# Kernel tuning notes

Hardware: AMD Instinct MI355X
Metric: run time of the kernel (lower is better)

The kernel has to match this reference:

```python
import jax, jax.numpy as jnp
import numpy as np

B, NX, C, KX = 16, 8192, 128, 16  # batch, grid size, channels, retained positive modes


def setup_inputs() -> dict:
    key = jax.random.key(0)
    k1, k2, k3 = jax.random.split(key, 3)
    x = jax.random.normal(k1, (B, NX, C), dtype=jnp.float32)
    scale = 1.0 / (C ** 2)
    w_real = scale * jax.random.uniform(k2, (KX + 1, C, C), dtype=jnp.float32)
    w_imag = scale * jax.random.uniform(k3, (KX + 1, C, C), dtype=jnp.float32)
    return {"x": x, "w_real": w_real, "w_imag": w_imag}


def reference(x, w_real, w_imag):
    # x: (b, nx, c); weights: (kx+1, c, c) complex
    nx = x.shape[1]
    k1 = w_real.shape[0]  # kx + 1 retained frequencies
    w = w_real + 1j * w_imag
    fx = jnp.fft.rfft(x, axis=-2)  # (b, nx//2+1, c) complex
    # torch.matmul(weights, fx[:, :kx+1, :, None])[..., 0]:
    # out[b,k,i] = sum_j w[k,i,j] * fx[b,k,j]
    out_ft = jnp.einsum('kij,bkj->bki', w, fx[:, :k1, :])
    # zero-pad truncated spectrum back to full rfft length, then inverse
    pad = nx // 2 + 1 - k1
    out_full = jnp.pad(out_ft, ((0, 0), (0, pad), (0, 0)))
    return jnp.fft.irfft(out_full, n=nx, axis=-2)
```

## Files before the change

kernel.cpp:

```cpp
#include <hip/hip_runtime.h>
#include <math.h>

#define B_     16
#define NX_    8192
#define C_     128
#define K1_    17
#define KP_    18
#define NC_    64
#define NH_    4096

typedef float v2f __attribute__((ext_vector_type(2)));
typedef float v4f __attribute__((ext_vector_type(4)));

#define GPART_F ((size_t)B_ * K1_ * 2 * NC_ * C_)

__global__ __launch_bounds__(256) void k_fwd(const float* __restrict__ x,
                                             float* __restrict__ ws) {
    __shared__ v4f smem[2 * 64 * 19];

    float* gpart = ws;
    const int b = blockIdx.y;
    const int c = blockIdx.x;
    const int t = threadIdx.x;
    const int jq  = t & 31;
    const int sub = (t >> 5) & 1;
    const int w   = t >> 6;
    const int i0  = c * 64;

    {
        float2* tg = (float2*)smem;
        for (int idx = t; idx < 64 * KP_; idx += 256) {
            int i = idx / KP_;
            int k = idx - i * KP_;
            float2 v = make_float2(0.f, 0.f);
            if (k < K1_) {
                int m = (k * (i0 + i)) & (NX_ - 1);
                float rev = (float)m * (1.0f / (float)NX_);
                v = make_float2(__builtin_amdgcn_cosf(rev),
                                __builtin_amdgcn_sinf(rev));
            }
            tg[idx] = v;
        }
    }
    __syncthreads();

    v4f gr[9], gs[9];
#pragma unroll
    for (int kk = 0; kk < 9; ++kk) { gr[kk] = (v4f)(0.f); gs[kk] = (v4f)(0.f); }

    const size_t xb = (size_t)b * NX_ * C_;
    const int ibase = w * 16;
    const float2* tp = (const float2*)smem + (size_t)ibase * KP_ + sub * 9;
    const float* xlo_p = x + xb + (size_t)(i0 + ibase) * C_ + 4 * jq;
    const float* xhi_p = x + xb + (size_t)(NX_ - (i0 + ibase)) * C_ + 4 * jq;

#pragma unroll 4
    for (int s = 0; s < 16; ++s) {
        const int nlo = i0 + ibase + s;
        v4f xlo = *(const v4f*)(xlo_p + (size_t)s * C_);
        v4f xhi = (v4f)(0.f);
        if (nlo > 0)
            xhi = *(const v4f*)(xhi_p - (size_t)s * C_);
        v4f xp = xlo + xhi;
        v4f xm = xlo - xhi;
        const float2* tr = tp + (size_t)s * KP_;
#pragma unroll
        for (int kk = 0; kk < 9; ++kk) {
            float2 tt = tr[kk];
            gr[kk] = __builtin_elementwise_fma(xp, (v4f)(tt.x), gr[kk]);
            gs[kk] = __builtin_elementwise_fma(xm, (v4f)(tt.y), gs[kk]);
        }
    }

    if (c == 0 && w == 0) {
        v4f x4 = *(const v4f*)(x + xb + (size_t)NH_ * C_ + 4 * jq);
#pragma unroll
        for (int kk = 0; kk < 9; ++kk) {
            int k = sub * 9 + kk;
            gr[kk] += (k & 1) ? -x4 : x4;
        }
    }

    const int lid = t & 63;
    __syncthreads();
    if (w >= 2) {
        v4f* p = smem + ((size_t)(w - 2) * 64 + lid) * 19;
#pragma unroll
        for (int kk = 0; kk < 9; ++kk) { p[2 * kk] = gr[kk]; p[2 * kk + 1] = gs[kk]; }
    }
    __syncthreads();
    if (w < 2) {
        const v4f* p = smem + ((size_t)w * 64 + lid) * 19;
#pragma unroll
        for (int kk = 0; kk < 9; ++kk) { gr[kk] += p[2 * kk]; gs[kk] += p[2 * kk + 1]; }
    }
    __syncthreads();
    if (w == 1) {
        v4f* p = smem + (size_t)lid * 19;
#pragma unroll
        for (int kk = 0; kk < 9; ++kk) { p[2 * kk] = gr[kk]; p[2 * kk + 1] = gs[kk]; }
    }
    __syncthreads();
    if (w == 0) {
        const v4f* p = smem + (size_t)lid * 19;
#pragma unroll
        for (int kk = 0; kk < 9; ++kk) {
            gr[kk] += p[2 * kk];
            gs[kk] += p[2 * kk + 1];
            int k = sub * 9 + kk;
            if (k < K1_) {
                float* gpR = gpart + ((((size_t)b * K1_ + k) * 2 + 0) * NC_ + c) * C_ + 4 * jq;
                float* gpS = gpart + ((((size_t)b * K1_ + k) * 2 + 1) * NC_ + c) * C_ + 4 * jq;
                *(v4f*)gpR = gr[kk];
                *(v4f*)gpS = gs[kk];
            }
        }
    }
}

__global__ __launch_bounds__(1024) void k_mix(const float* __restrict__ wr_g,
                                              const float* __restrict__ wi_g,
                                              float* __restrict__ ws) {
    const int k = blockIdx.x;
    const int b = blockIdx.y;
    const int t = threadIdx.x;

    const float* gpart = ws;
    float2* acoef = (float2*)(ws + GPART_F);

    __shared__ float part[8][C_];
    __shared__ float gsum[2][C_];
    __shared__ float hp[16][C_];

    {
        const int ch = t & 127, ri = (t >> 7) & 1, sh = t >> 8;
        const float* base = gpart
            + (((size_t)b * K1_ + k) * 2 + ri) * ((size_t)NC_ * C_) + ch;
        float g = 0.f;
#pragma unroll
        for (int s = 0; s < 16; ++s) g += base[(size_t)(sh * 16 + s) * C_];
        part[sh * 2 + ri][ch] = g;
    }
    __syncthreads();
    if (t < 256) {
        const int ch = t & 127, ri = t >> 7;
        gsum[ri][ch] = part[ri][ch] + part[2 + ri][ch]
                     + part[4 + ri][ch] + part[6 + ri][ch];
    }
    __syncthreads();

    {
        const int i = t & 127, q = t >> 7;
        float hr = 0.f, hi = 0.f;
        const float* wrp = wr_g + ((size_t)k * C_ + i) * C_;
        const float* wip = wi_g + ((size_t)k * C_ + i) * C_;
#pragma unroll
        for (int jjj = 0; jjj < 16; ++jjj) {
            int jj = q * 16 + jjj;
            float wr = wrp[jj], wi = wip[jj];
            float a = gsum[0][jj], cc = gsum[1][jj];
            hr = fmaf(wr, a, hr); hr = fmaf( wi, cc, hr);
            hi = fmaf(wi, a, hi); hi = fmaf(-wr, cc, hi);
        }
        hp[q * 2 + 0][i] = hr;
        hp[q * 2 + 1][i] = hi;
    }
    __syncthreads();
    if (t < 128) {
        const int i = t;
        float hr = 0.f, hi = 0.f;
#pragma unroll
        for (int q = 0; q < 8; ++q) { hr += hp[q * 2][i]; hi += hp[q * 2 + 1][i]; }
        float cf = (k == 0 ? 1.0f : 2.0f) / (float)NX_;
        acoef[((size_t)b * K1_ + k) * C_ + i] = make_float2(cf * hr, -cf * hi);
    }
}

__global__ __launch_bounds__(256) void k_inv(float* __restrict__ out,
                                             const float* __restrict__ ws) {
    __shared__ float2 smem[64 * K1_];

    const float4* acoef4 = (const float4*)(ws + GPART_F);
    const int b = blockIdx.y;
    const int c = blockIdx.x;
    const int t = threadIdx.x;
    const int jp = t & 63;
    const int h = t >> 6;
    const int i0 = c * 64;

    for (int idx = t; idx < 64 * K1_; idx += 256) {
        int i = idx / K1_;
        int k = idx - i * K1_;
        int m = (k * (i0 + i)) & (NX_ - 1);
        float rev = (float)m * (1.0f / (float)NX_);
        smem[idx] = make_float2(__builtin_amdgcn_cosf(rev),
                                __builtin_amdgcn_sinf(rev));
    }

    v2f arP[K1_], aiP[K1_];
#pragma unroll
    for (int k = 0; k < K1_; ++k) {
        float4 a = acoef4[((size_t)b * K1_ + k) * (C_ / 2) + jp];
        arP[k] = (v2f){a.x, a.z};
        aiP[k] = (v2f){a.y, a.w};
    }
    __syncthreads();

    const size_t ob = (size_t)b * NX_ * C_;
    const float2* tl = smem + (size_t)h * 16 * K1_;
#pragma unroll 4
    for (int s = 0; s < 16; ++s) {
        const int nlo = i0 + h * 16 + s;
        const float2* tr = tl + s * K1_;
        v2f S1 = (v2f)(0.f), S2 = (v2f)(0.f);
#pragma unroll
        for (int k = 0; k < K1_; ++k) {
            float2 tt = tr[k];
            v2f cc = {tt.x, tt.x};
            v2f ss = {tt.y, tt.y};
            S1 = __builtin_elementwise_fma(arP[k], cc, S1);
            S2 = __builtin_elementwise_fma(aiP[k], ss, S2);
        }
        *(v2f*)(out + ob + (size_t)nlo * C_ + 2 * jp) = S1 + S2;
        if (nlo > 0)
            *(v2f*)(out + ob + (size_t)(NX_ - nlo) * C_ + 2 * jp) = S1 - S2;
    }

    if (c == 0 && h == 0) {
        v2f o = (v2f)(0.f);
#pragma unroll
        for (int k = 0; k < K1_; ++k) o += (k & 1) ? -arP[k] : arP[k];
        *(v2f*)(out + ob + (size_t)NH_ * C_ + 2 * jp) = o;
    }
}

extern "C" void kernel_launch(void* const* d_in, const int* in_sizes, int n_in,
                              void* d_out, int out_size, void* d_ws, size_t ws_size,
                              hipStream_t stream) {
    const float* x  = (const float*)d_in[0];
    const float* wr = (const float*)d_in[1];
    const float* wi = (const float*)d_in[2];
    float* out = (float*)d_out;
    float* ws  = (float*)d_ws;

    k_fwd<<<dim3(NC_, B_), 256, 0, stream>>>(x, ws);
    k_mix<<<dim3(K1_, B_), 1024, 0, stream>>>(wr, wi, ws);
    k_inv<<<dim3(NC_, B_), 256, 0, stream>>>(out, ws);
}
```

Measured before the change: 52.90 us.

## Use half-period even/odd mode symmetry instead of mirror symmetry in forward and inverse DFT

The forward and inverse DFT kernels now pair position n with n+NX/2 instead of n with NX-n. Even modes see x[n]+x[n+NX/2] and odd modes see x[n]-x[n+NX/2], so each thread does a single sign-folded combine of two rows and uses the same input for both cos and sin accumulations. The twiddle table is reordered into even/odd mode groups. This removes the nlo>0 branch and the special Nyquist-row fixups, and the stores and loads become contiguous forward strides. The FMA count per element is unchanged, and the mode indexing on write-out is more complex.

```diff
diff --git a/kernel.cpp b/kernel.cpp
--- a/kernel.cpp
+++ b/kernel.cpp
@@ -31,9 +31,10 @@
         float2* tg = (float2*)smem;
         for (int idx = t; idx < 64 * KP_; idx += 256) {
             int i = idx / KP_;
-            int k = idx - i * KP_;
+            int p = idx - i * KP_;
             float2 v = make_float2(0.f, 0.f);
-            if (k < K1_) {
+            if (p < K1_) {
+                int k = (p < 9) ? 2 * p : 2 * (p - 9) + 1;
                 int m = (k * (i0 + i)) & (NX_ - 1);
                 float rev = (float)m * (1.0f / (float)NX_);
                 v = make_float2(__builtin_amdgcn_cosf(rev),
@@ -50,34 +51,22 @@
 
     const size_t xb = (size_t)b * NX_ * C_;
     const int ibase = w * 16;
+    const float sg = sub ? -1.f : 1.f;
     const float2* tp = (const float2*)smem + (size_t)ibase * KP_ + sub * 9;
     const float* xlo_p = x + xb + (size_t)(i0 + ibase) * C_ + 4 * jq;
-    const float* xhi_p = x + xb + (size_t)(NX_ - (i0 + ibase)) * C_ + 4 * jq;
+    const float* xhi_p = xlo_p + (size_t)NH_ * C_;
 
 #pragma unroll 4
     for (int s = 0; s < 16; ++s) {
-        const int nlo = i0 + ibase + s;
         v4f xlo = *(const v4f*)(xlo_p + (size_t)s * C_);
-        v4f xhi = (v4f)(0.f);
-        if (nlo > 0)
-            xhi = *(const v4f*)(xhi_p - (size_t)s * C_);
-        v4f xp = xlo + xhi;
-        v4f xm = xlo - xhi;
+        v4f xhi = *(const v4f*)(xhi_p + (size_t)s * C_);
+        v4f xs = __builtin_elementwise_fma(xhi, (v4f)(sg), xlo);
         const float2* tr = tp + (size_t)s * KP_;
 #pragma unroll
         for (int kk = 0; kk < 9; ++kk) {
             float2 tt = tr[kk];
-            gr[kk] = __builtin_elementwise_fma(xp, (v4f)(tt.x), gr[kk]);
-            gs[kk] = __builtin_elementwise_fma(xm, (v4f)(tt.y), gs[kk]);
-        }
-    }
-
-    if (c == 0 && w == 0) {
-        v4f x4 = *(const v4f*)(x + xb + (size_t)NH_ * C_ + 4 * jq);
-#pragma unroll
-        for (int kk = 0; kk < 9; ++kk) {
-            int k = sub * 9 + kk;
-            gr[kk] += (k & 1) ? -x4 : x4;
+            gr[kk] = __builtin_elementwise_fma(xs, (v4f)(tt.x), gr[kk]);
+            gs[kk] = __builtin_elementwise_fma(xs, (v4f)(tt.y), gs[kk]);
         }
     }
 
@@ -107,8 +96,8 @@
         for (int kk = 0; kk < 9; ++kk) {
             gr[kk] += p[2 * kk];
             gs[kk] += p[2 * kk + 1];
-            int k = sub * 9 + kk;
-            if (k < K1_) {
+            if (sub == 0 || kk < 8) {
+                int k = sub ? 2 * kk + 1 : 2 * kk;
                 float* gpR = gpart + ((((size_t)b * K1_ + k) * 2 + 0) * NC_ + c) * C_ + 4 * jq;
                 float* gpS = gpart + ((((size_t)b * K1_ + k) * 2 + 1) * NC_ + c) * C_ + 4 * jq;
                 *(v4f*)gpR = gr[kk];
@@ -208,29 +197,27 @@
 
     const size_t ob = (size_t)b * NX_ * C_;
     const float2* tl = smem + (size_t)h * 16 * K1_;
+    float* olo = out + ob + (size_t)(i0 + h * 16) * C_ + 2 * jp;
+    float* ohi = olo + (size_t)NH_ * C_;
 #pragma unroll 4
     for (int s = 0; s < 16; ++s) {
-        const int nlo = i0 + h * 16 + s;
         const float2* tr = tl + s * K1_;
-        v2f S1 = (v2f)(0.f), S2 = (v2f)(0.f);
+        v2f Se = (v2f)(0.f), So = (v2f)(0.f);
 #pragma unroll
         for (int k = 0; k < K1_; ++k) {
             float2 tt = tr[k];
             v2f cc = {tt.x, tt.x};
             v2f ss = {tt.y, tt.y};
-            S1 = __builtin_elementwise_fma(arP[k], cc, S1);
-            S2 = __builtin_elementwise_fma(aiP[k], ss, S2);
-        }
-        *(v2f*)(out + ob + (size_t)nlo * C_ + 2 * jp) = S1 + S2;
-        if (nlo > 0)
-            *(v2f*)(out + ob + (size_t)(NX_ - nlo) * C_ + 2 * jp) = S1 - S2;
-    }
-
-    if (c == 0 && h == 0) {
-        v2f o = (v2f)(0.f);
-#pragma unroll
-        for (int k = 0; k < K1_; ++k) o += (k & 1) ? -arP[k] : arP[k];
-        *(v2f*)(out + ob + (size_t)NH_ * C_ + 2 * jp) = o;
+            if ((k & 1) == 0) {
+                Se = __builtin_elementwise_fma(arP[k], cc, Se);
+                Se = __builtin_elementwise_fma(aiP[k], ss, Se);
+            } else {
+                So = __builtin_elementwise_fma(arP[k], cc, So);
+                So = __builtin_elementwise_fma(aiP[k], ss, So);
+            }
+        }
+        *(v2f*)(olo + (size_t)s * C_) = Se + So;
+        *(v2f*)(ohi + (size_t)s * C_) = Se - So;
     }
 }
 
```

Measured after the change: 51.76 us. 1.02x faster.
